# Kernel tuning notes

Hardware: AMD Instinct MI355X
Metric: run time of the kernel (lower is better)

## Reference

```python
import jax, jax.numpy as jnp
import numpy as np

K = 1.0  # distance scale from __init__


def setup_inputs() -> dict:
    key = jax.random.key(0)
    k1, k2, k3 = jax.random.split(key, 3)
    x_tilde = jax.random.normal(k1, (2048, 128), dtype=jnp.float32)
    X = jax.random.normal(k2, (100000, 128), dtype=jnp.float32)
    w = jax.random.normal(k3, (100000, 1), dtype=jnp.float32) * 0.1
    return {"x_tilde": x_tilde, "X": X, "w": w, "k": 10}


def reference(x_tilde, X, w, k):
    # w' = sqrt((max(relu(w)) - w) / K), shape [n, 1]  (get_w_prime)
    w_prime = jnp.sqrt((jnp.max(jax.nn.relu(w)) - w) / K)
    wp2 = jnp.squeeze(w_prime, 1) ** 2  # [n]

    # Exact L2 search over augmented vectors [X, w'] vs [x_tilde, 0]:
    # squared dist = ||q - x_n||^2 + w'_n^2  (FAISS IndexFlatL2 returns squared L2)
    q2 = jnp.sum(x_tilde * x_tilde, axis=1, keepdims=True)        # [B,1]
    x2 = jnp.sum(X * X, axis=1)                                    # [n]
    d2 = q2 - 2.0 * (x_tilde @ X.T) + x2[None, :] + wp2[None, :]   # [B,n]

    neg_D, I = jax.lax.top_k(-d2, k)  # k smallest distances
    D = -neg_D                         # [B,k] approximated (squared) activations

    # get_actual_distances: ||x_i - x|| = sqrt(relu(D - w'[I]^2))
    D_actual = jnp.sqrt(jax.nn.relu(D - wp2[I]))  # [B,k]

    # get_maximal_neighbor_activations: f_i = w[I] - K * ||x_i - x||, argmax over k
    f = jnp.squeeze(w, 1)[I] - K * D_actual  # [B,k]
    j = jnp.argmax(f, axis=1)                # [B]
    rows = jnp.arange(f.shape[0])
    D_out = f[rows, j]                       # [B]
    I_out = I[rows, j]                       # [B] database indices
    return D_out, I_out
```

## Files before the change

kernel.cpp:

```cpp
#include <hip/hip_runtime.h>
#include <stdint.h>

typedef short   shortx8 __attribute__((ext_vector_type(8)));
typedef float   f32x4   __attribute__((ext_vector_type(4)));

#define CPS 16

static __device__ __forceinline__ unsigned short f2bf(float f) {
  unsigned u = __float_as_uint(f);
  unsigned r = u + 0x7FFFu + ((u >> 16) & 1u);
  return (unsigned short)(r >> 16);
}

static __device__ __forceinline__ void gl2lds16(const void* gsrc, void* ldst) {
  __builtin_amdgcn_global_load_lds(
      (const __attribute__((address_space(1))) unsigned int*)gsrc,
      (__attribute__((address_space(3))) unsigned int*)ldst, 16, 0, 0);
}

__global__ void k_prep(const float* __restrict__ X, const float* __restrict__ xt,
                       const float* __restrict__ w, unsigned short* __restrict__ xb,
                       unsigned short* __restrict__ qb, float* __restrict__ aug,
                       float* __restrict__ q2, int n, int npad, int xblocks, int B) {
  const int wv = threadIdx.x >> 6, lane = threadIdx.x & 63;
  if ((int)blockIdx.x < xblocks) {
    int r = blockIdx.x * 4 + wv;
    if (r >= npad) return;
    if (r < n) {
      float2 v = *(const float2*)(X + (size_t)r * 128 + lane * 2);
      unsigned pk = (unsigned)f2bf(v.x) | ((unsigned)f2bf(v.y) << 16);
      *(unsigned*)(xb + (size_t)r * 128 + lane * 2) = pk;
      float s = v.x * v.x + v.y * v.y;
      for (int m = 32; m; m >>= 1) s += __shfl_xor(s, m);
      if (lane == 0) aug[r] = s - w[r];
    } else {
      *(unsigned*)(xb + (size_t)r * 128 + lane * 2) = 0;
      if (lane == 0) aug[r] = 1e30f;
    }
  } else {
    int r = (blockIdx.x - xblocks) * 4 + wv;
    if (r >= B) return;
    float2 v = *(const float2*)(xt + (size_t)r * 128 + lane * 2);
    unsigned pk = (unsigned)f2bf(v.x) | ((unsigned)f2bf(v.y) << 16);
    *(unsigned*)(qb + (size_t)r * 128 + lane * 2) = pk;
    float s = v.x * v.x + v.y * v.y;
    for (int m = 32; m; m >>= 1) s += __shfl_xor(s, m);
    if (lane == 0) q2[r] = s;
  }
}

__global__ __launch_bounds__(256, 2) void k_gemm(const unsigned short* __restrict__ qb,
    const unsigned short* __restrict__ xb, const float* __restrict__ aug,
    float* __restrict__ cmin, int C) {
  __shared__ __align__(16) unsigned short tile[2][8192];
  const int S = C / CPS;
  const int b = blockIdx.x;
  const int xcd = b & 7;
  const int j = b >> 3;
  const int sj = j % 13, xq = j / 13;
  const int qq = S >> 3, rr = S & 7;
  const int nst = (xcd < rr) ? (qq + 1) : qq;
  if (sj >= nst) return;
  const int ystripe = (xcd < rr) ? (xcd * (qq + 1) + sj)
                                 : (rr * (qq + 1) + (xcd - rr) * qq + sj);
  const int c0 = ystripe * CPS;

  const int t = threadIdx.x;
  const int lane = t & 63, wv = t >> 6;
  const int li = lane & 15, lg = lane >> 4;
  const int qbase = xq * 256 + wv * 64;

  shortx8 qf[4][4];
#pragma unroll
  for (int qt = 0; qt < 4; ++qt)
#pragma unroll
    for (int ks = 0; ks < 4; ++ks)
      qf[qt][ks] = *(const shortx8*)(qb + (size_t)(qbase + qt * 16 + li) * 128 + ks * 32 + lg * 8);

  int soff[4];
#pragma unroll
  for (int jj = 0; jj < 4; ++jj) {
    int o = wv * 4096 + jj * 1024 + lane * 16;
    int r = o >> 8;
    soff[jj] = (o & ~255) | ((o & 255) ^ ((r & 7) << 4));
  }

#define STAGE(buf, cc) do {                                                  \
    const char* _s = (const char*)xb + (size_t)(cc) * 16384;                 \
    _Pragma("unroll")                                                        \
    for (int _j = 0; _j < 4; ++_j)                                           \
      gl2lds16(_s + soff[_j], &tile[buf][wv * 2048 + _j * 512]);             \
  } while (0)

  float cm[4][4];
#pragma unroll
  for (int qt = 0; qt < 4; ++qt)
#pragma unroll
    for (int jj = 0; jj < 4; ++jj) cm[qt][jj] = 1e38f;

  f32x4 av[2][4];
#pragma unroll
  for (int rg = 0; rg < 4; ++rg)
    av[0][rg] = *(const f32x4*)(aug + (size_t)c0 * 64 + rg * 16 + lg * 4);

  STAGE(0, c0);
  __syncthreads();

#pragma unroll
  for (int cc = 0; cc < CPS; ++cc) {
    const int cur = cc & 1;
    if (cc + 1 < CPS) {
      STAGE(cur ^ 1, c0 + cc + 1);
#pragma unroll
      for (int rg = 0; rg < 4; ++rg)
        av[cur ^ 1][rg] = *(const f32x4*)(aug + (size_t)(c0 + cc + 1) * 64 + rg * 16 + lg * 4);
    }

    f32x4 acc[4][4];
#pragma unroll
    for (int rg = 0; rg < 4; ++rg)
#pragma unroll
      for (int qt = 0; qt < 4; ++qt)
        acc[rg][qt] = (f32x4){0.f, 0.f, 0.f, 0.f};

#pragma unroll
    for (int rg = 0; rg < 4; ++rg) {
      const int r = rg * 16 + li;
      const int rsw = (r & 7) << 3;
      shortx8 af[4];
#pragma unroll
      for (int ks = 0; ks < 4; ++ks)
        af[ks] = *(const shortx8*)(&tile[cur][r * 128 + ((ks * 32 + lg * 8) ^ rsw)]);
#pragma unroll
      for (int qt = 0; qt < 4; ++qt)
#pragma unroll
        for (int ks = 0; ks < 4; ++ks)
          acc[rg][qt] = __builtin_amdgcn_mfma_f32_16x16x32_bf16(af[ks], qf[qt][ks], acc[rg][qt], 0, 0, 0);
    }

    float m[4];
#pragma unroll
    for (int qt = 0; qt < 4; ++qt) {
      float v = 1e38f;
#pragma unroll
      for (int rg = 0; rg < 4; ++rg)
#pragma unroll
        for (int p = 0; p < 4; ++p)
          v = fminf(v, fmaf(-2.f, acc[rg][qt][p], av[cur][rg][p]));
      v = fminf(v, __shfl_xor(v, 16));
      v = fminf(v, __shfl_xor(v, 32));
      m[qt] = v;
    }
#pragma unroll
    for (int qt = 0; qt < 4; ++qt)
      cm[qt][cc >> 2] = (lg == (cc & 3)) ? m[qt] : cm[qt][cc >> 2];

    __syncthreads();
  }
#undef STAGE

  float* outf = (float*)tile;
#pragma unroll
  for (int qt = 0; qt < 4; ++qt)
#pragma unroll
    for (int jj = 0; jj < 4; ++jj)
      outf[(wv * 64 + qt * 16 + li) * 20 + jj * 4 + lg] = cm[qt][jj];
  __syncthreads();
#pragma unroll
  for (int p = 0; p < 4; ++p) {
    int flat = p * 1024 + t * 4;
    int ql = flat >> 4, cix = flat & 15;
    f32x4 v = *(const f32x4*)&outf[ql * 20 + cix];
    *(f32x4*)&cmin[(size_t)(xq * 256 + ql) * C + c0 + cix] = v;
  }
}

__global__ void k_tau(const float* __restrict__ cmin, float* __restrict__ tau,
                      const int* __restrict__ kptr, int* __restrict__ ccnt,
                      int* __restrict__ clist, int C, int B) {
  __shared__ float arr[1600];
  __shared__ float red[4];
  __shared__ int   redi[4];
  __shared__ float bval;
  __shared__ int   bidx;
  const int q = blockIdx.x, t = threadIdx.x;
  const int lane = t & 63, wv = t >> 6;
  const float* row = cmin + (size_t)q * C;
  float lmd = 1e38f; int lmi = -1;
  for (int i = t; i < C; i += 256) {
    float v = row[i]; arr[i] = v;
    if (v < lmd) { lmd = v; lmi = i; }
  }
  __syncthreads();
  int k = *kptr; if (k < 1) k = 1; if (k > 32) k = 32;
  float tv = 1e38f;
  for (int r = 0; r < k; ++r) {
    float md = lmd; int mi = lmi;
    for (int msk = 32; msk; msk >>= 1) {
      float od = __shfl_xor(md, msk); int oi = __shfl_xor(mi, msk);
      if (od < md) { md = od; mi = oi; }
    }
    if (lane == 0) { red[wv] = md; redi[wv] = mi; }
    __syncthreads();
    if (t == 0) {
      float bm = red[0]; int bi = redi[0];
      for (int u = 1; u < 4; ++u) if (red[u] < bm) { bm = red[u]; bi = redi[u]; }
      bval = bm; bidx = bi;
    }
    __syncthreads();
    tv = bval;
    const int sel = bidx;
    if (r + 1 < k && sel >= 0 && (sel & 255) == t) {
      arr[sel] = 1e38f;
      lmd = 1e38f; lmi = -1;
      for (int i = t; i < C; i += 256) {
        float v = arr[i];
        if (v < lmd) { lmd = v; lmi = i; }
      }
    }
    __syncthreads();
  }
  const float tq = tv + 1.5f;
  if (t == 0) tau[q] = tq;
  for (int i = t; i < C; i += 256)
    if (row[i] <= tq) {
      int pos = atomicAdd(&ccnt[i], 1);
      clist[(size_t)i * B + pos] = q;
    }
}

__global__ __launch_bounds__(256) void k_exact(const float* __restrict__ X, const float* __restrict__ xt,
    const float* __restrict__ aug, const float* __restrict__ q2, const float* __restrict__ tau,
    const int* __restrict__ ccnt, const int* __restrict__ clist,
    int* __restrict__ qcnt, float2* __restrict__ cand, int n, int B) {
  const int c = blockIdx.x;
  const int nq = ccnt[c];
  if (nq == 0) return;
  __shared__ float xs[64 * 128];
  __shared__ float qs[4 * 512];
  const int t = threadIdx.x, lane = t & 63, wv = t >> 6;
#pragma unroll
  for (int p = 0; p < 8; ++p) {
    int flat = p * 1024 + t * 4;
    int r = flat >> 7, col = flat & 127;
    long g = (long)c * 64 + r;
    f32x4 v = (f32x4){0.f, 0.f, 0.f, 0.f};
    if (g < n) v = *(const f32x4*)(X + g * 128 + col);
    *(f32x4*)&xs[r * 128 + ((((col >> 2) ^ (r & 31))) << 2)] = v;
  }
  const int gcol = c * 64 + lane;
  const float augv = aug[gcol];
  __syncthreads();

  float* qsw = qs + wv * 512;
  const int sw = lane & 31;
  const int su = (lane >> 4) & 3;
  const int scol = (lane & 15) * 8;
  for (int i0 = wv * 4; i0 < nq; i0 += 16) {
    const size_t cb = (size_t)c * B;
    int qn0 = __builtin_amdgcn_readfirstlane(clist[cb + min(i0 + 0, nq - 1)]);
    int qn1 = __builtin_amdgcn_readfirstlane(clist[cb + min(i0 + 1, nq - 1)]);
    int qn2 = __builtin_amdgcn_readfirstlane(clist[cb + min(i0 + 2, nq - 1)]);
    int qn3 = __builtin_amdgcn_readfirstlane(clist[cb + min(i0 + 3, nq - 1)]);
    {
      int qnu = (su == 0) ? qn0 : (su == 1) ? qn1 : (su == 2) ? qn2 : qn3;
      const float* Q = xt + (size_t)qnu * 128 + scol;
      *(f32x4*)&qsw[su * 128 + scol]     = *(const f32x4*)(Q);
      *(f32x4*)&qsw[su * 128 + scol + 4] = *(const f32x4*)(Q + 4);
    }
    float t0 = tau[qn0], t1 = tau[qn1], t2 = tau[qn2], t3 = tau[qn3];
    float g0 = q2[qn0], g1 = q2[qn1], g2 = q2[qn2], g3 = q2[qn3];
    float a0 = 0.f, a1 = 0.f, a2 = 0.f, a3 = 0.f;
#pragma unroll 4
    for (int jj = 0; jj < 32; ++jj) {
      f32x4 xv = *(const f32x4*)&xs[lane * 128 + ((jj ^ sw) << 2)];
      f32x4 v0 = *(const f32x4*)&qsw[0 * 128 + jj * 4];
      f32x4 v1 = *(const f32x4*)&qsw[1 * 128 + jj * 4];
      f32x4 v2 = *(const f32x4*)&qsw[2 * 128 + jj * 4];
      f32x4 v3 = *(const f32x4*)&qsw[3 * 128 + jj * 4];
#pragma unroll
      for (int e = 0; e < 4; ++e) {
        a0 = fmaf(xv[e], v0[e], a0);
        a1 = fmaf(xv[e], v1[e], a1);
        a2 = fmaf(xv[e], v2[e], a2);
        a3 = fmaf(xv[e], v3[e], a3);
      }
    }
#pragma unroll
    for (int u = 0; u < 4; ++u) {
      const float accv = (u == 0) ? a0 : (u == 1) ? a1 : (u == 2) ? a2 : a3;
      const int qnu   = (u == 0) ? qn0 : (u == 1) ? qn1 : (u == 2) ? qn2 : qn3;
      const float tuu = (u == 0) ? t0 : (u == 1) ? t1 : (u == 2) ? t2 : t3;
      const float g2u = (u == 0) ? g0 : (u == 1) ? g1 : (u == 2) ? g2 : g3;
      const float s = fmaf(-2.f, accv, augv);
      if ((i0 + u) < nq && gcol < n && s <= tuu) {
        int pos = atomicAdd(&qcnt[qnu], 1);
        if (pos < 256) {
          float d2v = fmaf(-2.f, accv, g2u) + augv;
          cand[(size_t)qnu * 256 + pos] = make_float2(d2v, __int_as_float(gcol));
        }
      }
    }
  }
}

__global__ void k_final(const float* __restrict__ w,
    const float2* __restrict__ cand, const int* __restrict__ qcnt, const int* __restrict__ kptr,
    float* __restrict__ dout, int B, int n) {
  const int q = blockIdx.x, lane = threadIdx.x;
  int k = *kptr; if (k < 1) k = 1; if (k > 64) k = 64;
  const int cnt = min(qcnt[q], 256);
  float d0 = 1e38f, d1 = 1e38f, d2v = 1e38f, d3 = 1e38f;
  int i0 = 0x7fffffff, i1 = 0x7fffffff, i2 = 0x7fffffff, i3 = 0x7fffffff;
  {
    int s;
    s = lane;       if (s < cnt) { float2 cc = cand[(size_t)q * 256 + s]; d0 = cc.x; i0 = __float_as_int(cc.y); }
    s = lane + 64;  if (s < cnt) { float2 cc = cand[(size_t)q * 256 + s]; d1 = cc.x; i1 = __float_as_int(cc.y); }
    s = lane + 128; if (s < cnt) { float2 cc = cand[(size_t)q * 256 + s]; d2v = cc.x; i2 = __float_as_int(cc.y); }
    s = lane + 192; if (s < cnt) { float2 cc = cand[(size_t)q * 256 + s]; d3 = cc.x; i3 = __float_as_int(cc.y); }
  }
  float bestf = -1e38f; int besti = 0;
  for (int r = 0; r < k; ++r) {
    float md = d0; int mi = i0; int mj = 0;
    if (d1 < md || (d1 == md && i1 < mi)) { md = d1; mi = i1; mj = 1; }
    if (d2v < md || (d2v == md && i2 < mi)) { md = d2v; mi = i2; mj = 2; }
    if (d3 < md || (d3 == md && i3 < mi)) { md = d3; mi = i3; mj = 3; }
    int ml = lane;
    for (int msk = 32; msk; msk >>= 1) {
      float od = __shfl_xor(md, msk); int oi = __shfl_xor(mi, msk);
      int ol = __shfl_xor(ml, msk);   int oj = __shfl_xor(mj, msk);
      if (od < md || (od == md && oi < mi)) { md = od; mi = oi; ml = ol; mj = oj; }
    }
    if (lane == ml) {
      if (mj == 0)      { d0 = 1e38f;  i0 = 0x7fffffff; }
      else if (mj == 1) { d1 = 1e38f;  i1 = 0x7fffffff; }
      else if (mj == 2) { d2v = 1e38f; i2 = 0x7fffffff; }
      else              { d3 = 1e38f;  i3 = 0x7fffffff; }
    }
    if (mi >= 0 && mi < n) {
      float wi = w[mi];
      float da = sqrtf(fmaxf(md + wi, 0.f));
      float f = wi - da;
      if (f > bestf) { bestf = f; besti = mi; }
    }
  }
  if (lane == 0) { dout[q] = bestf; dout[B + q] = (float)besti; }
}

extern "C" void kernel_launch(void* const* d_in, const int* in_sizes, int n_in,
                              void* d_out, int out_size, void* d_ws, size_t ws_size,
                              hipStream_t stream) {
  const float* xt = (const float*)d_in[0];
  const float* X  = (const float*)d_in[1];
  const float* w  = (const float*)d_in[2];
  const int* kptr = (const int*)d_in[3];
  const int B = in_sizes[0] / 128;
  const int n = in_sizes[2];
  const int C = ((n + 63) / 64 + CPS - 1) / CPS * CPS;
  const int npad = C * 64;

  char* ws = (char*)d_ws;
  const size_t o_ccnt = 0;
  const size_t o_qcnt = 8192;
  const size_t o_q2   = 16384;
  const size_t o_tau  = o_q2 + (size_t)B * 4;
  const size_t o_aug  = o_tau + (size_t)B * 4;
  const size_t o_cmin = (o_aug + (size_t)npad * 4 + 255) & ~(size_t)255;
  const size_t o_clist= (o_cmin + (size_t)B * C * 4 + 255) & ~(size_t)255;
  const size_t o_cand = (o_clist + (size_t)C * B * 4 + 255) & ~(size_t)255;
  const size_t o_qb   = (o_cand + (size_t)B * 256 * 8 + 255) & ~(size_t)255;
  const size_t o_xb   = (o_qb + (size_t)B * 128 * 2 + 255) & ~(size_t)255;

  int* ccnt  = (int*)(ws + o_ccnt);
  int* qcnt  = (int*)(ws + o_qcnt);
  float* q2  = (float*)(ws + o_q2);
  float* tau = (float*)(ws + o_tau);
  float* aug = (float*)(ws + o_aug);
  float* cmin = (float*)(ws + o_cmin);
  int* clist = (int*)(ws + o_clist);
  float2* cand = (float2*)(ws + o_cand);
  unsigned short* qb = (unsigned short*)(ws + o_qb);
  unsigned short* xb = (unsigned short*)(ws + o_xb);

  hipMemsetAsync(d_ws, 0, 16384, stream);

  const int xblocks = npad / 4;
  k_prep<<<xblocks + B / 4, 256, 0, stream>>>(X, xt, w, xb, qb, aug, q2, n, npad, xblocks, B);

  k_gemm<<<832, 256, 0, stream>>>(qb, xb, aug, cmin, C);

  k_tau<<<B, 256, 0, stream>>>(cmin, tau, kptr, ccnt, clist, C, B);
  k_exact<<<C, 256, 0, stream>>>(X, xt, aug, q2, tau, ccnt, clist, qcnt, cand, n, B);
  k_final<<<B, 64, 0, stream>>>(w, cand, qcnt, kptr, (float*)d_out, B, n);
}
```

Baseline: 231.6 us.

## Triple-buffer GEMM tiles, halve chunks per block, stage aug in LDS, widen prep

The distance GEMM moves from a double-buffered to a triple-buffered LDS pipeline. It waits with explicit vmcnt and barriers in place of a full syncthreads per chunk, and raises MFMA priority with setprio. Chunks per block drop from 16 to 8, so the grid grows to 1600 blocks with occupancy hint 3, and aug values are staged once into LDS. The prep kernel processes two rows per wave with 16-byte loads. The goal is better load/compute overlap and more parallelism, at the cost of more LDS per block and more partial-min writes.

```diff
diff --git a/kernel.cpp b/kernel.cpp
--- a/kernel.cpp
+++ b/kernel.cpp
@@ -4,7 +4,7 @@
 typedef short   shortx8 __attribute__((ext_vector_type(8)));
 typedef float   f32x4   __attribute__((ext_vector_type(4)));
 
-#define CPS 16
+#define CPS 8
 
 static __device__ __forceinline__ unsigned short f2bf(float f) {
   unsigned u = __float_as_uint(f);
@@ -22,42 +22,43 @@
                        const float* __restrict__ w, unsigned short* __restrict__ xb,
                        unsigned short* __restrict__ qb, float* __restrict__ aug,
                        float* __restrict__ q2, int n, int npad, int xblocks, int B) {
-  const int wv = threadIdx.x >> 6, lane = threadIdx.x & 63;
+  const int hw = threadIdx.x >> 5;
+  const int hl = threadIdx.x & 31;
+  const int col = hl * 4;
   if ((int)blockIdx.x < xblocks) {
-    int r = blockIdx.x * 4 + wv;
-    if (r >= npad) return;
+    int r = blockIdx.x * 8 + hw;
     if (r < n) {
-      float2 v = *(const float2*)(X + (size_t)r * 128 + lane * 2);
-      unsigned pk = (unsigned)f2bf(v.x) | ((unsigned)f2bf(v.y) << 16);
-      *(unsigned*)(xb + (size_t)r * 128 + lane * 2) = pk;
-      float s = v.x * v.x + v.y * v.y;
-      for (int m = 32; m; m >>= 1) s += __shfl_xor(s, m);
-      if (lane == 0) aug[r] = s - w[r];
+      f32x4 v = *(const f32x4*)(X + (size_t)r * 128 + col);
+      ushort4 us = make_ushort4(f2bf(v[0]), f2bf(v[1]), f2bf(v[2]), f2bf(v[3]));
+      *(ushort4*)(xb + (size_t)r * 128 + col) = us;
+      float s = v[0] * v[0] + v[1] * v[1] + v[2] * v[2] + v[3] * v[3];
+      for (int m = 16; m; m >>= 1) s += __shfl_xor(s, m);
+      if (hl == 0) aug[r] = s - w[r];
     } else {
-      *(unsigned*)(xb + (size_t)r * 128 + lane * 2) = 0;
-      if (lane == 0) aug[r] = 1e30f;
+      *(ushort4*)(xb + (size_t)r * 128 + col) = make_ushort4(0, 0, 0, 0);
+      if (hl == 0) aug[r] = 1e30f;
     }
   } else {
-    int r = (blockIdx.x - xblocks) * 4 + wv;
-    if (r >= B) return;
-    float2 v = *(const float2*)(xt + (size_t)r * 128 + lane * 2);
-    unsigned pk = (unsigned)f2bf(v.x) | ((unsigned)f2bf(v.y) << 16);
-    *(unsigned*)(qb + (size_t)r * 128 + lane * 2) = pk;
-    float s = v.x * v.x + v.y * v.y;
-    for (int m = 32; m; m >>= 1) s += __shfl_xor(s, m);
-    if (lane == 0) q2[r] = s;
-  }
-}
-
-__global__ __launch_bounds__(256, 2) void k_gemm(const unsigned short* __restrict__ qb,
+    int r = (blockIdx.x - xblocks) * 8 + hw;
+    f32x4 v = *(const f32x4*)(xt + (size_t)r * 128 + col);
+    ushort4 us = make_ushort4(f2bf(v[0]), f2bf(v[1]), f2bf(v[2]), f2bf(v[3]));
+    *(ushort4*)(qb + (size_t)r * 128 + col) = us;
+    float s = v[0] * v[0] + v[1] * v[1] + v[2] * v[2] + v[3] * v[3];
+    for (int m = 16; m; m >>= 1) s += __shfl_xor(s, m);
+    if (hl == 0) q2[r] = s;
+  }
+}
+
+__global__ __launch_bounds__(256, 3) void k_gemm(const unsigned short* __restrict__ qb,
     const unsigned short* __restrict__ xb, const float* __restrict__ aug,
     float* __restrict__ cmin, int C) {
-  __shared__ __align__(16) unsigned short tile[2][8192];
+  __shared__ __align__(16) unsigned short tile[3][8192];
+  __shared__ __align__(16) float augs[CPS * 64];
   const int S = C / CPS;
   const int b = blockIdx.x;
   const int xcd = b & 7;
   const int j = b >> 3;
-  const int sj = j % 13, xq = j / 13;
+  const int sj = j % 25, xq = j / 25;
   const int qq = S >> 3, rr = S & 7;
   const int nst = (xcd < rr) ? (qq + 1) : qq;
   if (sj >= nst) return;
@@ -77,6 +78,11 @@
     for (int ks = 0; ks < 4; ++ks)
       qf[qt][ks] = *(const shortx8*)(qb + (size_t)(qbase + qt * 16 + li) * 128 + ks * 32 + lg * 8);
 
+  {
+    float2 a2 = *(const float2*)(aug + (size_t)c0 * 64 + t * 2);
+    *(float2*)&augs[t * 2] = a2;
+  }
+
   int soff[4];
 #pragma unroll
   for (int jj = 0; jj < 4; ++jj) {
@@ -92,29 +98,24 @@
       gl2lds16(_s + soff[_j], &tile[buf][wv * 2048 + _j * 512]);             \
   } while (0)
 
-  float cm[4][4];
+  float cm[4][2];
 #pragma unroll
   for (int qt = 0; qt < 4; ++qt)
 #pragma unroll
-    for (int jj = 0; jj < 4; ++jj) cm[qt][jj] = 1e38f;
-
-  f32x4 av[2][4];
-#pragma unroll
-  for (int rg = 0; rg < 4; ++rg)
-    av[0][rg] = *(const f32x4*)(aug + (size_t)c0 * 64 + rg * 16 + lg * 4);
-
+    for (int jj = 0; jj < 2; ++jj) cm[qt][jj] = 1e38f;
+
+  __syncthreads();
   STAGE(0, c0);
-  __syncthreads();
+  STAGE(1, c0 + 1);
 
 #pragma unroll
   for (int cc = 0; cc < CPS; ++cc) {
-    const int cur = cc & 1;
-    if (cc + 1 < CPS) {
-      STAGE(cur ^ 1, c0 + cc + 1);
-#pragma unroll
-      for (int rg = 0; rg < 4; ++rg)
-        av[cur ^ 1][rg] = *(const f32x4*)(aug + (size_t)(c0 + cc + 1) * 64 + rg * 16 + lg * 4);
-    }
+    const int cur = cc % 3;
+    if (cc < CPS - 1) asm volatile("s_waitcnt vmcnt(4)" ::: "memory");
+    else              asm volatile("s_waitcnt vmcnt(0)" ::: "memory");
+    __builtin_amdgcn_s_barrier();
+    __builtin_amdgcn_sched_barrier(0);
+    if (cc + 2 < CPS) STAGE((cc + 2) % 3, c0 + cc + 2);
 
     f32x4 acc[4][4];
 #pragma unroll
@@ -123,6 +124,7 @@
       for (int qt = 0; qt < 4; ++qt)
         acc[rg][qt] = (f32x4){0.f, 0.f, 0.f, 0.f};
 
+    __builtin_amdgcn_s_setprio(1);
 #pragma unroll
     for (int rg = 0; rg < 4; ++rg) {
       const int r = rg * 16 + li;
@@ -137,16 +139,19 @@
         for (int ks = 0; ks < 4; ++ks)
           acc[rg][qt] = __builtin_amdgcn_mfma_f32_16x16x32_bf16(af[ks], qf[qt][ks], acc[rg][qt], 0, 0, 0);
     }
+    __builtin_amdgcn_s_setprio(0);
 
     float m[4];
 #pragma unroll
     for (int qt = 0; qt < 4; ++qt) {
       float v = 1e38f;
 #pragma unroll
-      for (int rg = 0; rg < 4; ++rg)
+      for (int rg = 0; rg < 4; ++rg) {
+        f32x4 avv = *(const f32x4*)&augs[cc * 64 + rg * 16 + lg * 4];
 #pragma unroll
         for (int p = 0; p < 4; ++p)
-          v = fminf(v, fmaf(-2.f, acc[rg][qt][p], av[cur][rg][p]));
+          v = fminf(v, fmaf(-2.f, acc[rg][qt][p], avv[p]));
+      }
       v = fminf(v, __shfl_xor(v, 16));
       v = fminf(v, __shfl_xor(v, 32));
       m[qt] = v;
@@ -154,23 +159,22 @@
 #pragma unroll
     for (int qt = 0; qt < 4; ++qt)
       cm[qt][cc >> 2] = (lg == (cc & 3)) ? m[qt] : cm[qt][cc >> 2];
-
-    __syncthreads();
   }
 #undef STAGE
 
+  __syncthreads();
   float* outf = (float*)tile;
 #pragma unroll
   for (int qt = 0; qt < 4; ++qt)
 #pragma unroll
-    for (int jj = 0; jj < 4; ++jj)
-      outf[(wv * 64 + qt * 16 + li) * 20 + jj * 4 + lg] = cm[qt][jj];
-  __syncthreads();
-#pragma unroll
-  for (int p = 0; p < 4; ++p) {
+    for (int jj = 0; jj < 2; ++jj)
+      outf[(wv * 64 + qt * 16 + li) * 12 + jj * 4 + lg] = cm[qt][jj];
+  __syncthreads();
+#pragma unroll
+  for (int p = 0; p < 2; ++p) {
     int flat = p * 1024 + t * 4;
-    int ql = flat >> 4, cix = flat & 15;
-    f32x4 v = *(const f32x4*)&outf[ql * 20 + cix];
+    int ql = flat >> 3, cix = flat & 7;
+    f32x4 v = *(const f32x4*)&outf[ql * 12 + cix];
     *(f32x4*)&cmin[(size_t)(xq * 256 + ql) * C + c0 + cix] = v;
   }
 }
@@ -384,10 +388,10 @@
 
   hipMemsetAsync(d_ws, 0, 16384, stream);
 
-  const int xblocks = npad / 4;
-  k_prep<<<xblocks + B / 4, 256, 0, stream>>>(X, xt, w, xb, qb, aug, q2, n, npad, xblocks, B);
-
-  k_gemm<<<832, 256, 0, stream>>>(qb, xb, aug, cmin, C);
+  const int xblocks = npad / 8;
+  k_prep<<<xblocks + B / 8, 256, 0, stream>>>(X, xt, w, xb, qb, aug, q2, n, npad, xblocks, B);
+
+  k_gemm<<<1600, 256, 0, stream>>>(qb, xb, aug, cmin, C);
 
   k_tau<<<B, 256, 0, stream>>>(cmin, tau, kptr, ccnt, clist, C, B);
   k_exact<<<C, 256, 0, stream>>>(X, xt, aug, q2, tau, ccnt, clist, qcnt, cand, n, B);
```

Result: faster. 226.1 us (-2.4%).
